# Kernel optimization log

Hardware: AMD Instinct MI355X
Metric: run time of the kernel (lower is better)

The kernel has to match this reference:

```python
import jax, jax.numpy as jnp
import numpy as np

TAU_PRE = 2.0   # pre-synaptic trace time constant
SCALE = 1.0     # forward(scale=1.0) default
SPIKE_P = 0.1   # firing probability for realistic binary spike trains


def setup_inputs() -> dict:
    key = jax.random.key(0)
    k1, k2 = jax.random.split(key)
    T, B, NIN, NOUT = 2048, 128, 256, 128
    # binary spike trains, [T, B, N]
    in_spikes = (jax.random.uniform(k1, (T, B, NIN)) < SPIKE_P).astype(jnp.float32)
    out_spikes = (jax.random.uniform(k2, (T, B, NOUT)) < SPIKE_P).astype(jnp.float32)
    return {"in_spikes": in_spikes, "out_spikes": out_spikes}


def reference(in_spikes, out_spikes):
    # STDP.forward: loop over recorded timesteps, per step:
    #   trace_pre = trace_pre - trace_pre/tau_pre + in_spike          (decayed trace)
    #   dw = sum_b trace_pre[b, :] (outer) out_spike[b, :] -> [NOUT, NIN]
    #   delta_w += scale * dw
    # Expressed as a single lax.scan over the time axis.
    B, NIN = in_spikes.shape[1], in_spikes.shape[2]
    NOUT = out_spikes.shape[2]

    def step(carry, xs):
        trace_pre, delta_w = carry
        s_in, s_out = xs                                 # [B, NIN], [B, NOUT]
        trace_pre = trace_pre - trace_pre / TAU_PRE + s_in
        dw = jnp.einsum('bi,bo->oi', trace_pre, s_out)   # [NOUT, NIN]
        return (trace_pre, delta_w + SCALE * dw), None

    init = (jnp.zeros((B, NIN), in_spikes.dtype),
            jnp.zeros((NOUT, NIN), in_spikes.dtype))
    (_, delta_w), _ = jax.lax.scan(step, init, (in_spikes, out_spikes))
    return delta_w
```

## Files before the change

### kernel.cpp

```cpp
#include <hip/hip_runtime.h>
#include <hip/hip_bf16.h>

#define T_TOTAL 2048
#define BATCH   128
#define NIN     256
#define NOUT    128

#define TC      256
#define BC      4
#define WARM    32
#define G       4
#define NTC     (T_TOTAL / TC)
#define NBC     (BATCH / BC)
#define NBLOCKS (NTC * NBC)
#define NG      (TC / G)

#define ROWU      24
#define OUT_ELEMS (NOUT * NIN)

typedef __attribute__((ext_vector_type(8)))  __bf16 bf16x8;
typedef __attribute__((ext_vector_type(2)))  __bf16 bf16x2;
typedef __attribute__((ext_vector_type(16))) float  f32x16;

static __device__ __forceinline__ unsigned pack_bf16(float a, float b) {
    bf16x2 v = { (__bf16)a, (__bf16)b };
    union { bf16x2 v; unsigned u; } c; c.v = v; return c.u;
}

__global__ __launch_bounds__(512, 2)
void stdp_main(const float* __restrict__ in, const float* __restrict__ outs,
               float* __restrict__ dst, int nslots, int use_atomic)
{
    __shared__ unsigned short tr_lds[2][NIN * ROWU];
    __shared__ unsigned short ot_lds[2][NOUT * ROWU];

    const int tid = threadIdx.x;
    const int bc  = blockIdx.x % NBC;
    const int tc  = blockIdx.x / NBC;
    const int b0  = bc * BC;
    const int t0  = tc * TC;

    const int i_idx = tid & 255;
    const int bh    = tid >> 8;
    const int o_idx = tid & 127;
    const int blo   = (tid >> 7) & 3;

    float tr0 = 0.f, tr1 = 0.f;

    if (tc > 0) {
        for (int t = t0 - WARM; t < t0; t += 8) {
            float v0[8], v1[8];
#pragma unroll
            for (int u = 0; u < 8; ++u) {
                const size_t base = ((size_t)(t + u) * BATCH + b0 + 2 * bh) * NIN + i_idx;
                v0[u] = in[base];
                v1[u] = in[base + NIN];
            }
#pragma unroll
            for (int u = 0; u < 8; ++u) {
                tr0 = 0.5f * tr0 + v0[u];
                tr1 = 0.5f * tr1 + v1[u];
            }
        }
    }

    f32x16 acc[4];
#pragma unroll
    for (int j = 0; j < 4; ++j) acc[j] = (f32x16)(0.f);

    const int lane  = tid & 63;
    const int wv    = tid >> 6;
    const int mt    = wv & 3;
    const int ntb   = (wv >> 2) * 4;
    const int l31   = lane & 31;
    const int khalf = lane >> 5;

    float P0[2][G], P1[2][G], PO[2][G];

    auto load_stage = [&](int s, int g) {
        const int tg = t0 + g * G;
#pragma unroll
        for (int q = 0; q < G; ++q) {
            const size_t baseI = ((size_t)(tg + q) * BATCH + b0 + 2 * bh) * NIN + i_idx;
            P0[s][q] = in[baseI];
            P1[s][q] = in[baseI + NIN];
            PO[s][q] = outs[((size_t)(tg + q) * BATCH + b0 + blo) * NOUT + o_idx];
        }
    };

    auto body = [&](int s, int g) {
        unsigned words[G];
        __bf16 ob[G];
#pragma unroll
        for (int q = 0; q < G; ++q) {
            tr0 = 0.5f * tr0 + P0[s][q];
            tr1 = 0.5f * tr1 + P1[s][q];
            words[q] = pack_bf16(tr0, tr1);
            ob[q] = (__bf16)PO[s][q];
        }
        if (g + 2 < NG) load_stage(s, g + 2);

        unsigned* trow = (unsigned*)&tr_lds[s][i_idx * ROWU];
#pragma unroll
        for (int q = 0; q < G; ++q) trow[q * 2 + bh] = words[q];
        __bf16* orow = (__bf16*)&ot_lds[s][o_idx * ROWU];
#pragma unroll
        for (int q = 0; q < G; ++q) orow[q * 4 + blo] = ob[q];

        __syncthreads();

        const bf16x8 a = *(const bf16x8*)&ot_lds[s][(mt * 32 + l31) * ROWU + khalf * 8];
#pragma unroll
        for (int j = 0; j < 4; ++j) {
            const bf16x8 b = *(const bf16x8*)&tr_lds[s][((ntb + j) * 32 + l31) * ROWU + khalf * 8];
            acc[j] = __builtin_amdgcn_mfma_f32_32x32x16_bf16(a, b, acc[j], 0, 0, 0);
        }
    };

    load_stage(0, 0);
    load_stage(1, 1);
    for (int gg = 0; gg < NG; gg += 2) {
        body(0, gg);
        body(1, gg + 1);
    }

    float* base = dst + (size_t)(use_atomic ? (blockIdx.x % nslots) : blockIdx.x) * OUT_ELEMS;
#pragma unroll
    for (int j = 0; j < 4; ++j) {
        const int icol = (ntb + j) * 32 + l31;
#pragma unroll
        for (int r = 0; r < 16; ++r) {
            const int row = (r & 3) + 8 * (r >> 2) + 4 * khalf;
            const int o   = mt * 32 + row;
            const float v = acc[j][r];
            if (use_atomic) atomicAdd(&base[o * NIN + icol], v);
            else            base[o * NIN + icol] = v;
        }
    }
}

__global__ void zero_kernel(float* p, int n) {
    int i = blockIdx.x * blockDim.x + threadIdx.x;
    if (i < n) p[i] = 0.f;
}

__global__ __launch_bounds__(256)
void reduce_kernel(const float* __restrict__ ws, float* __restrict__ outp, int nslots) {
    const int idx = blockIdx.x * 256 + threadIdx.x;
    float s = 0.f;
    int k = 0;
    for (; k + 16 <= nslots; k += 16) {
        float v[16];
#pragma unroll
        for (int u = 0; u < 16; ++u) v[u] = ws[(size_t)(k + u) * OUT_ELEMS + idx];
#pragma unroll
        for (int u = 0; u < 16; ++u) s += v[u];
    }
    for (; k < nslots; ++k) s += ws[(size_t)k * OUT_ELEMS + idx];
    outp[idx] = s;
}

extern "C" void kernel_launch(void* const* d_in, const int* in_sizes, int n_in,
                              void* d_out, int out_size, void* d_ws, size_t ws_size,
                              hipStream_t stream) {
    const float* in   = (const float*)d_in[0];
    const float* outs = (const float*)d_in[1];
    float* out = (float*)d_out;
    float* ws  = (float*)d_ws;

    const size_t slot_bytes = (size_t)OUT_ELEMS * sizeof(float);

    if (ws_size >= (size_t)NBLOCKS * slot_bytes) {
        stdp_main<<<NBLOCKS, 512, 0, stream>>>(in, outs, ws, NBLOCKS, 0);
        reduce_kernel<<<OUT_ELEMS / 256, 256, 0, stream>>>(ws, out, NBLOCKS);
    } else if (ws_size >= 16 * slot_bytes) {
        zero_kernel<<<(16 * OUT_ELEMS + 255) / 256, 256, 0, stream>>>(ws, 16 * OUT_ELEMS);
        stdp_main<<<NBLOCKS, 512, 0, stream>>>(in, outs, ws, 16, 1);
        reduce_kernel<<<OUT_ELEMS / 256, 256, 0, stream>>>(ws, out, 16);
    } else {
        zero_kernel<<<(OUT_ELEMS + 255) / 256, 256, 0, stream>>>(out, OUT_ELEMS);
        stdp_main<<<NBLOCKS, 512, 0, stream>>>(in, outs, out, 1, 1);
    }
}
```

Measured before the change: 450.9 us.

## Process 16 timesteps per barrier with XOR-swizzled 128-bit LDS staging

Each barrier now covers a super-step of 16 timesteps instead of 4, cutting the number of __syncthreads by four and issuing four MFMAs per j per barrier. LDS rows widen to 32 words with an XOR swizzle, so trace and output-spike data are written and read as 128-bit vectors without bank conflicts. The out-spike loads are repartitioned so each thread packs two batch rows across 8 timesteps. The explicit two-stage register prefetch is dropped, so global loads now sit on the critical path unless the compiler and the two resident blocks hide their latency. Register pressure also rises from the 16-deep load arrays.

```diff
diff --git a/kernel.cpp b/kernel.cpp
--- a/kernel.cpp
+++ b/kernel.cpp
@@ -9,18 +9,18 @@
 #define TC      256
 #define BC      4
 #define WARM    32
-#define G       4
 #define NTC     (T_TOTAL / TC)
 #define NBC     (BATCH / BC)
 #define NBLOCKS (NTC * NBC)
-#define NG      (TC / G)
+#define SUP     16
+#define NSUP    (TC / SUP)
 
-#define ROWU      24
 #define OUT_ELEMS (NOUT * NIN)
 
 typedef __attribute__((ext_vector_type(8)))  __bf16 bf16x8;
 typedef __attribute__((ext_vector_type(2)))  __bf16 bf16x2;
 typedef __attribute__((ext_vector_type(16))) float  f32x16;
+typedef __attribute__((ext_vector_type(4)))  unsigned uint32x4;
 
 static __device__ __forceinline__ unsigned pack_bf16(float a, float b) {
     bf16x2 v = { (__bf16)a, (__bf16)b };
@@ -31,8 +31,8 @@
 void stdp_main(const float* __restrict__ in, const float* __restrict__ outs,
                float* __restrict__ dst, int nslots, int use_atomic)
 {
-    __shared__ unsigned short tr_lds[2][NIN * ROWU];
-    __shared__ unsigned short ot_lds[2][NOUT * ROWU];
+    __shared__ __align__(16) unsigned tr_lds[2][NIN * 32];
+    __shared__ __align__(16) unsigned ot_lds[2][NOUT * 32];
 
     const int tid = threadIdx.x;
     const int bc  = blockIdx.x % NBC;
@@ -43,7 +43,8 @@
     const int i_idx = tid & 255;
     const int bh    = tid >> 8;
     const int o_idx = tid & 127;
-    const int blo   = (tid >> 7) & 3;
+    const int bp    = (tid >> 7) & 1;
+    const int th    = (tid >> 8) & 1;
 
     float tr0 = 0.f, tr1 = 0.f;
 
@@ -74,54 +75,67 @@
     const int ntb   = (wv >> 2) * 4;
     const int l31   = lane & 31;
     const int khalf = lane >> 5;
+    const int sw    = l31 & 7;
 
-    float P0[2][G], P1[2][G], PO[2][G];
+    for (int sg = 0; sg < NSUP; ++sg) {
+        const int ts  = t0 + sg * SUP;
+        const int buf = sg & 1;
 
-    auto load_stage = [&](int s, int g) {
-        const int tg = t0 + g * G;
+        float vin0[SUP], vin1[SUP];
 #pragma unroll
-        for (int q = 0; q < G; ++q) {
-            const size_t baseI = ((size_t)(tg + q) * BATCH + b0 + 2 * bh) * NIN + i_idx;
-            P0[s][q] = in[baseI];
-            P1[s][q] = in[baseI + NIN];
-            PO[s][q] = outs[((size_t)(tg + q) * BATCH + b0 + blo) * NOUT + o_idx];
+        for (int s = 0; s < SUP; ++s) {
+            const size_t base = ((size_t)(ts + s) * BATCH + b0 + 2 * bh) * NIN + i_idx;
+            vin0[s] = in[base];
+            vin1[s] = in[base + NIN];
         }
-    };
+        float vo0[8], vo1[8];
+#pragma unroll
+        for (int u = 0; u < 8; ++u) {
+            const size_t baseO = ((size_t)(ts + th * 8 + u) * BATCH + b0 + 2 * bp) * NOUT + o_idx;
+            vo0[u] = outs[baseO];
+            vo1[u] = outs[baseO + NOUT];
+        }
 
-    auto body = [&](int s, int g) {
-        unsigned words[G];
-        __bf16 ob[G];
 #pragma unroll
-        for (int q = 0; q < G; ++q) {
-            tr0 = 0.5f * tr0 + P0[s][q];
-            tr1 = 0.5f * tr1 + P1[s][q];
-            words[q] = pack_bf16(tr0, tr1);
-            ob[q] = (__bf16)PO[s][q];
+        for (int s16 = 0; s16 < 4; ++s16) {
+            unsigned bw[4];
+#pragma unroll
+            for (int q = 0; q < 4; ++q) {
+                const int s = s16 * 4 + q;
+                tr0 = 0.5f * tr0 + vin0[s];
+                tr1 = 0.5f * tr1 + vin1[s];
+                bw[q] = pack_bf16(tr0, tr1);
+            }
+            const int p = (s16 * 2 + bh) ^ (i_idx & 7);
+            *(uint32x4*)&tr_lds[buf][i_idx * 32 + p * 4] = (uint32x4){bw[0], bw[1], bw[2], bw[3]};
         }
-        if (g + 2 < NG) load_stage(s, g + 2);
 
-        unsigned* trow = (unsigned*)&tr_lds[s][i_idx * ROWU];
 #pragma unroll
-        for (int q = 0; q < G; ++q) trow[q * 2 + bh] = words[q];
-        __bf16* orow = (__bf16*)&ot_lds[s][o_idx * ROWU];
+        for (int e = 0; e < 2; ++e) {
+            const int s16 = th * 2 + e;
+            unsigned aw[4];
 #pragma unroll
-        for (int q = 0; q < G; ++q) orow[q * 4 + blo] = ob[q];
+            for (int q = 0; q < 4; ++q) {
+                const int u = e * 4 + q;
+                aw[q] = pack_bf16(vo0[u], vo1[u]);
+            }
+            const int p = (s16 * 2 + bp) ^ (o_idx & 7);
+            *(uint32x4*)&ot_lds[buf][o_idx * 32 + p * 4] = (uint32x4){aw[0], aw[1], aw[2], aw[3]};
+        }
 
         __syncthreads();
 
-        const bf16x8 a = *(const bf16x8*)&ot_lds[s][(mt * 32 + l31) * ROWU + khalf * 8];
 #pragma unroll
-        for (int j = 0; j < 4; ++j) {
-            const bf16x8 b = *(const bf16x8*)&tr_lds[s][((ntb + j) * 32 + l31) * ROWU + khalf * 8];
-            acc[j] = __builtin_amdgcn_mfma_f32_32x32x16_bf16(a, b, acc[j], 0, 0, 0);
+        for (int s16 = 0; s16 < 4; ++s16) {
+            const int pc = (s16 * 2 + khalf) ^ sw;
+            const bf16x8 a = *(const bf16x8*)&ot_lds[buf][(mt * 32 + l31) * 32 + pc * 4];
+#pragma unroll
+            for (int j = 0; j < 4; ++j) {
+                const int row = (ntb + j) * 32 + l31;
+                const bf16x8 b = *(const bf16x8*)&tr_lds[buf][row * 32 + pc * 4];
+                acc[j] = __builtin_amdgcn_mfma_f32_32x32x16_bf16(a, b, acc[j], 0, 0, 0);
+            }
         }
-    };
-
-    load_stage(0, 0);
-    load_stage(1, 1);
-    for (int gg = 0; gg < NG; gg += 2) {
-        body(0, gg);
-        body(1, gg + 1);
     }
 
     float* base = dst + (size_t)(use_atomic ? (blockIdx.x % nslots) : blockIdx.x) * OUT_ELEMS;
```

Measured after the change: 456.6 us. About the same (+1.3%).

## Build MFMA fragments directly in registers, removing LDS staging and barriers

Applied to the files above, without the earlier changes.

Each lane now computes one pre-synaptic trace and packs eight timesteps into a bf16 B fragment, with out-spike A fragments loaded straight from global memory, so the shared-memory transposes and per-step __syncthreads go away. The batch chunk per block is halved, doubling the block count and the number of partial slots that the reduce kernel must sum. The 16-slot atomic fallback is dropped. This trades barrier and LDS overhead for more redundant global loads and larger workspace traffic.

```diff
diff --git a/kernel.cpp b/kernel.cpp
--- a/kernel.cpp
+++ b/kernel.cpp
@@ -7,15 +7,16 @@
 #define NOUT    128
 
 #define TC      256
-#define BC      4
+#define NTC     (T_TOTAL / TC)
+#define BC      2
+#define NBP     (BATCH / BC)
+#define NBLOCKS (NBP * NTC)
 #define WARM    32
-#define G       4
-#define NTC     (T_TOTAL / TC)
-#define NBC     (BATCH / BC)
-#define NBLOCKS (NTC * NBC)
-#define NG      (TC / G)
+#define CT      8
+#define NCH     (TC / CT)
 
-#define ROWU      24
+#define STRI    (BATCH * NIN)
+#define STRO    (BATCH * NOUT)
 #define OUT_ELEMS (NOUT * NIN)
 
 typedef __attribute__((ext_vector_type(8)))  __bf16 bf16x8;
@@ -26,115 +27,109 @@
     bf16x2 v = { (__bf16)a, (__bf16)b };
     union { bf16x2 v; unsigned u; } c; c.v = v; return c.u;
 }
+static __device__ __forceinline__ bf16x8 frag4(unsigned w0, unsigned w1,
+                                               unsigned w2, unsigned w3) {
+    union { unsigned u[4]; bf16x8 f; } c;
+    c.u[0] = w0; c.u[1] = w1; c.u[2] = w2; c.u[3] = w3; return c.f;
+}
 
 __global__ __launch_bounds__(512, 2)
 void stdp_main(const float* __restrict__ in, const float* __restrict__ outs,
-               float* __restrict__ dst, int nslots, int use_atomic)
+               float* __restrict__ dst, int use_atomic)
 {
-    __shared__ unsigned short tr_lds[2][NIN * ROWU];
-    __shared__ unsigned short ot_lds[2][NOUT * ROWU];
+    const int tid  = threadIdx.x;
+    const int lane = tid & 63;
+    const int l31  = lane & 31;
+    const int kh   = lane >> 5;
+    const int nt   = tid >> 6;
 
-    const int tid = threadIdx.x;
-    const int bc  = blockIdx.x % NBC;
-    const int tc  = blockIdx.x / NBC;
-    const int b0  = bc * BC;
-    const int t0  = tc * TC;
+    const int tc = blockIdx.x & 7;
+    const int bp = blockIdx.x >> 3;
+    const int b0 = bp * BC;
+    const int t0 = tc * TC;
 
-    const int i_idx = tid & 255;
-    const int bh    = tid >> 8;
-    const int o_idx = tid & 127;
-    const int blo   = (tid >> 7) & 3;
+    const size_t in_off = (size_t)(b0 + kh) * NIN + nt * 32 + l31;
+    const size_t ot_off = (size_t)(b0 + kh) * NOUT + l31;
 
-    float tr0 = 0.f, tr1 = 0.f;
+    float tr = 0.f;
 
     if (tc > 0) {
         for (int t = t0 - WARM; t < t0; t += 8) {
-            float v0[8], v1[8];
+            float v[8];
 #pragma unroll
-            for (int u = 0; u < 8; ++u) {
-                const size_t base = ((size_t)(t + u) * BATCH + b0 + 2 * bh) * NIN + i_idx;
-                v0[u] = in[base];
-                v1[u] = in[base + NIN];
-            }
+            for (int u = 0; u < 8; ++u) v[u] = in[(size_t)(t + u) * STRI + in_off];
 #pragma unroll
-            for (int u = 0; u < 8; ++u) {
-                tr0 = 0.5f * tr0 + v0[u];
-                tr1 = 0.5f * tr1 + v1[u];
-            }
+            for (int u = 0; u < 8; ++u) tr = 0.5f * tr + v[u];
         }
     }
 
     f32x16 acc[4];
 #pragma unroll
-    for (int j = 0; j < 4; ++j) acc[j] = (f32x16)(0.f);
+    for (int m = 0; m < 4; ++m) acc[m] = (f32x16)(0.f);
 
-    const int lane  = tid & 63;
-    const int wv    = tid >> 6;
-    const int mt    = wv & 3;
-    const int ntb   = (wv >> 2) * 4;
-    const int l31   = lane & 31;
-    const int khalf = lane >> 5;
+    float cin[8];
+#pragma unroll
+    for (int j = 0; j < 8; ++j) cin[j] = in[(size_t)(t0 + j) * STRI + in_off];
 
-    float P0[2][G], P1[2][G], PO[2][G];
+    for (int c = 0; c < NCH; ++c) {
+        const int tb = t0 + c * CT;
 
-    auto load_stage = [&](int s, int g) {
-        const int tg = t0 + g * G;
+        float af[4][8];
 #pragma unroll
-        for (int q = 0; q < G; ++q) {
-            const size_t baseI = ((size_t)(tg + q) * BATCH + b0 + 2 * bh) * NIN + i_idx;
-            P0[s][q] = in[baseI];
-            P1[s][q] = in[baseI + NIN];
-            PO[s][q] = outs[((size_t)(tg + q) * BATCH + b0 + blo) * NOUT + o_idx];
+        for (int m = 0; m < 4; ++m)
+#pragma unroll
+            for (int j = 0; j < 8; ++j)
+                af[m][j] = outs[(size_t)(tb + j) * STRO + ot_off + m * 32];
+
+        float nin[8];
+        if (c + 1 < NCH) {
+#pragma unroll
+            for (int j = 0; j < 8; ++j) nin[j] = in[(size_t)(tb + CT + j) * STRI + in_off];
         }
-    };
 
-    auto body = [&](int s, int g) {
-        unsigned words[G];
-        __bf16 ob[G];
+        unsigned bw[4];
 #pragma unroll
-        for (int q = 0; q < G; ++q) {
-            tr0 = 0.5f * tr0 + P0[s][q];
-            tr1 = 0.5f * tr1 + P1[s][q];
-            words[q] = pack_bf16(tr0, tr1);
-            ob[q] = (__bf16)PO[s][q];
+        for (int p = 0; p < 4; ++p) {
+            tr = 0.5f * tr + cin[2 * p];
+            const float f0 = tr;
+            tr = 0.5f * tr + cin[2 * p + 1];
+            bw[p] = pack_bf16(f0, tr);
         }
-        if (g + 2 < NG) load_stage(s, g + 2);
+        const bf16x8 bfrag = frag4(bw[0], bw[1], bw[2], bw[3]);
 
-        unsigned* trow = (unsigned*)&tr_lds[s][i_idx * ROWU];
 #pragma unroll
-        for (int q = 0; q < G; ++q) trow[q * 2 + bh] = words[q];
-        __bf16* orow = (__bf16*)&ot_lds[s][o_idx * ROWU];
+        for (int m = 0; m < 4; ++m) {
+            const bf16x8 afrag = frag4(pack_bf16(af[m][0], af[m][1]),
+                                       pack_bf16(af[m][2], af[m][3]),
+                                       pack_bf16(af[m][4], af[m][5]),
+                                       pack_bf16(af[m][6], af[m][7]));
+            acc[m] = __builtin_amdgcn_mfma_f32_32x32x16_bf16(afrag, bfrag, acc[m], 0, 0, 0);
+        }
+
 #pragma unroll
-        for (int q = 0; q < G; ++q) orow[q * 4 + blo] = ob[q];
-
-        __syncthreads();
-
-        const bf16x8 a = *(const bf16x8*)&ot_lds[s][(mt * 32 + l31) * ROWU + khalf * 8];
-#pragma unroll
-        for (int j = 0; j < 4; ++j) {
-            const bf16x8 b = *(const bf16x8*)&tr_lds[s][((ntb + j) * 32 + l31) * ROWU + khalf * 8];
-            acc[j] = __builtin_amdgcn_mfma_f32_32x32x16_bf16(a, b, acc[j], 0, 0, 0);
-        }
-    };
-
-    load_stage(0, 0);
-    load_stage(1, 1);
-    for (int gg = 0; gg < NG; gg += 2) {
-        body(0, gg);
-        body(1, gg + 1);
+        for (int j = 0; j < 8; ++j) cin[j] = nin[j];
     }
 
-    float* base = dst + (size_t)(use_atomic ? (blockIdx.x % nslots) : blockIdx.x) * OUT_ELEMS;
+    if (use_atomic) {
 #pragma unroll
-    for (int j = 0; j < 4; ++j) {
-        const int icol = (ntb + j) * 32 + l31;
+        for (int m = 0; m < 4; ++m) {
+            const int icol = nt * 32 + l31;
 #pragma unroll
-        for (int r = 0; r < 16; ++r) {
-            const int row = (r & 3) + 8 * (r >> 2) + 4 * khalf;
-            const int o   = mt * 32 + row;
-            const float v = acc[j][r];
-            if (use_atomic) atomicAdd(&base[o * NIN + icol], v);
-            else            base[o * NIN + icol] = v;
+            for (int r = 0; r < 16; ++r) {
+                const int row = (r & 3) + 8 * (r >> 2) + 4 * kh;
+                atomicAdd(&dst[(m * 32 + row) * NIN + icol], acc[m][r]);
+            }
+        }
+    } else {
+        float* base = dst + (size_t)blockIdx.x * OUT_ELEMS;
+#pragma unroll
+        for (int m = 0; m < 4; ++m) {
+            const int icol = nt * 32 + l31;
+#pragma unroll
+            for (int r = 0; r < 16; ++r) {
+                const int row = (r & 3) + 8 * (r >> 2) + 4 * kh;
+                base[(m * 32 + row) * NIN + icol] = acc[m][r];
+            }
         }
     }
 }
@@ -145,18 +140,16 @@
 }
 
 __global__ __launch_bounds__(256)
-void reduce_kernel(const float* __restrict__ ws, float* __restrict__ outp, int nslots) {
+void reduce_kernel(const float* __restrict__ ws, float* __restrict__ outp) {
     const int idx = blockIdx.x * 256 + threadIdx.x;
     float s = 0.f;
-    int k = 0;
-    for (; k + 16 <= nslots; k += 16) {
+    for (int k = 0; k < NBLOCKS; k += 16) {
         float v[16];
 #pragma unroll
         for (int u = 0; u < 16; ++u) v[u] = ws[(size_t)(k + u) * OUT_ELEMS + idx];
 #pragma unroll
         for (int u = 0; u < 16; ++u) s += v[u];
     }
-    for (; k < nslots; ++k) s += ws[(size_t)k * OUT_ELEMS + idx];
     outp[idx] = s;
 }
 
@@ -168,17 +161,11 @@
     float* out = (float*)d_out;
     float* ws  = (float*)d_ws;
 
-    const size_t slot_bytes = (size_t)OUT_ELEMS * sizeof(float);
-
-    if (ws_size >= (size_t)NBLOCKS * slot_bytes) {
-        stdp_main<<<NBLOCKS, 512, 0, stream>>>(in, outs, ws, NBLOCKS, 0);
-        reduce_kernel<<<OUT_ELEMS / 256, 256, 0, stream>>>(ws, out, NBLOCKS);
-    } else if (ws_size >= 16 * slot_bytes) {
-        zero_kernel<<<(16 * OUT_ELEMS + 255) / 256, 256, 0, stream>>>(ws, 16 * OUT_ELEMS);
-        stdp_main<<<NBLOCKS, 512, 0, stream>>>(in, outs, ws, 16, 1);
-        reduce_kernel<<<OUT_ELEMS / 256, 256, 0, stream>>>(ws, out, 16);
+    if (ws_size >= (size_t)NBLOCKS * OUT_ELEMS * sizeof(float)) {
+        stdp_main<<<NBLOCKS, 512, 0, stream>>>(in, outs, ws, 0);
+        reduce_kernel<<<OUT_ELEMS / 256, 256, 0, stream>>>(ws, out);
     } else {
         zero_kernel<<<(OUT_ELEMS + 255) / 256, 256, 0, stream>>>(out, OUT_ELEMS);
-        stdp_main<<<NBLOCKS, 512, 0, stream>>>(in, outs, out, 1, 1);
+        stdp_main<<<NBLOCKS, 512, 0, stream>>>(in, outs, out, 1);
     }
 }
```

Measured after the change: 478.5 us. +6.1%, slower.
